# Kernel tuning notes

Measured on AMD Instinct MI355X. Metric: run time of the kernel, lower is better.

Reference implementation:

```python
import jax, jax.numpy as jnp
import numpy as np

B, T, D, H, O = 128, 1024, 256, 512, 256


def setup_inputs() -> dict:
    key = jax.random.key(0)
    ks = jax.random.split(key, 7)
    s = lambda k, shape, fan: jax.random.normal(k, shape, dtype=jnp.float32) / np.sqrt(fan)
    return {
        "x": jax.random.normal(ks[0], (B, T, D), dtype=jnp.float32),
        "W_ih": s(ks[1], (4 * H, D), D),
        "W_hh": s(ks[2], (4 * H, H), H),
        "b_ih": jnp.zeros((4 * H,), dtype=jnp.float32),
        "b_hh": jnp.zeros((4 * H,), dtype=jnp.float32),
        "W_out": s(ks[5], (O, H), H),
        "b_out": jnp.zeros((O,), dtype=jnp.float32),
    }


def reference(x, W_ih, W_hh, b_ih, b_hh, W_out, b_out):
    Bsz = x.shape[0]
    Hd = W_hh.shape[1]
    # Precompute input projections for all timesteps: [B, T, 4H]
    x_proj = jnp.einsum("btd,gd->btg", x, W_ih) + b_ih + b_hh

    def step(carry, xp_t):
        h, c = carry
        gates = xp_t + h @ W_hh.T  # [B, 4H]
        i, f, g, o = jnp.split(gates, 4, axis=-1)
        i = jax.nn.sigmoid(i)
        f = jax.nn.sigmoid(f)
        g = jnp.tanh(g)
        o = jax.nn.sigmoid(o)
        c = f * c + i * g
        h = o * jnp.tanh(c)
        return (h, c), None

    h0 = jnp.zeros((Bsz, Hd), dtype=x.dtype)
    c0 = jnp.zeros((Bsz, Hd), dtype=x.dtype)
    (h_T, _), _ = jax.lax.scan(step, (h0, c0), jnp.swapaxes(x_proj, 0, 1))
    return h_T @ W_out.T + b_out
```

## Files before the change

kernel.cpp:

```cpp
#include <hip/hip_runtime.h>

#define Bsz 128
#define Tlen 1024
#define Din 256
#define Hdim 512

#define NBG 8
#define NCG 16

typedef __attribute__((ext_vector_type(8))) short short8;
typedef __attribute__((ext_vector_type(4))) float f32x4;
typedef __attribute__((ext_vector_type(4))) unsigned short ushort4_;
typedef __attribute__((ext_vector_type(4))) unsigned int uint4v;

#define HBT_BYTES ((size_t)2 * NBG * 16 * Hdim * 4)
#define HT_OFF ((size_t)524288)
#define XB_OFF ((size_t)786432)
#define XB_BYTES ((size_t)Bsz * Tlen * Din * 2)

__device__ inline unsigned short f2bf(float f) {
    unsigned int u = __builtin_bit_cast(unsigned int, f);
    unsigned int lsb = (u >> 16) & 1u;
    u += 0x7fffu + lsb;
    return (unsigned short)(u >> 16);
}
__device__ inline float sigm_f(float x) { return 1.f / (1.f + __expf(-x)); }
__device__ inline float tanh_f(float x) { return 1.f - 2.f / (__expf(2.f * x) + 1.f); }

__device__ __forceinline__ bool chunk_ok(uint4v v, unsigned want) {
    unsigned m =
        ((v[0] ^ want) | (v[1] ^ want) | (v[2] ^ want) | (v[3] ^ want)) & 0xFFFFu;
    return m == 0;
}
__device__ __forceinline__ void chunk_to_lds(uint4v v, int c, unsigned char* h_lds) {
    int row = c >> 7;
    unsigned lo = (v[0] >> 16) | (v[1] & 0xFFFF0000u);
    unsigned hi = (v[2] >> 16) | (v[3] & 0xFFFF0000u);
    int a = ((row << 10) + ((c & 127) << 3)) ^ ((row & 7) << 4);
    *(unsigned long long*)(h_lds + a) =
        (unsigned long long)lo | ((unsigned long long)hi << 32);
}

__global__ __launch_bounds__(256) void xconv(const float* __restrict__ x,
                                             unsigned short* __restrict__ xb) {
    const size_t nthreads = (size_t)2048 * 256;
#pragma unroll
    for (int it = 0; it < 8; ++it) {
        size_t base =
            ((size_t)blockIdx.x * 256 + threadIdx.x + it * nthreads) * 8;
        float4 a = *(const float4*)(x + base);
        float4 b = *(const float4*)(x + base + 4);
        short8 o;
        o[0] = (short)f2bf(a.x); o[1] = (short)f2bf(a.y);
        o[2] = (short)f2bf(a.z); o[3] = (short)f2bf(a.w);
        o[4] = (short)f2bf(b.x); o[5] = (short)f2bf(b.y);
        o[6] = (short)f2bf(b.z); o[7] = (short)f2bf(b.w);
        *(short8*)(xb + base) = o;
    }
}

template <bool XB>
__global__ __launch_bounds__(512, 1) void lstm_persist_t(
    const float* __restrict__ x, const unsigned short* __restrict__ xb,
    const float* __restrict__ Wih, const float* __restrict__ Whh,
    const float* __restrict__ bih, const float* __restrict__ bhh,
    unsigned int* __restrict__ hbt, float* __restrict__ hT) {
    __shared__ unsigned char h_lds[16 * 1024];
    __shared__ unsigned char xh_lds[2 * 8192];
    __shared__ float gates_w[8][16 * 17];

    const int tid = threadIdx.x;
    const int bid = blockIdx.x;
    const int bg = bid & 7;
    const int cg = bid >> 3;
    const int lane = tid & 63;
    const int w = tid >> 6;
    const int n15 = lane & 15;
    const int k8 = lane >> 4;
    const int grow = bg * 16;
    const int gc = n15 & 3;
    const int gsel = n15 >> 2;
    const int myb = k8 * 4 + gsel;
    const int mycol = cg * 32 + w * 4 + gc;
    const int R = (n15 >> 2) * Hdim + mycol;

    short8 whh[16], wihh[8];
    {
        const float* wr = Whh + (size_t)R * Hdim;
#pragma unroll
        for (int kc = 0; kc < 16; kc++) {
            const float* p = wr + kc * 32 + k8 * 8;
            short8 f;
#pragma unroll
            for (int e = 0; e < 8; e++) f[e] = (short)f2bf(p[e]);
            whh[kc] = f;
        }
        const float* wr2 = Wih + (size_t)R * Din;
#pragma unroll
        for (int kc = 0; kc < 8; kc++) {
            const float* p = wr2 + kc * 32 + k8 * 8;
            short8 f;
#pragma unroll
            for (int e = 0; e < 8; e++) f[e] = (short)f2bf(p[e]);
            wihh[kc] = f;
        }
    }
    float bias4[4];
#pragma unroll
    for (int g = 0; g < 4; g++) bias4[g] = bih[g * Hdim + mycol] + bhh[g * Hdim + mycol];

    const int xrow = XB ? (tid >> 5) : 0;
    const int xc8 = XB ? (tid & 31) : 0;
    short8 xr8;
    float4 xrf[2];

    if (XB) {
        const unsigned short* xrowp = xb + ((size_t)(grow + xrow) * Tlen) * Din;
        short8 v = *(const short8*)(xrowp + (size_t)0 * Din + xc8 * 8);
        int a = ((xrow << 9) + (xc8 << 4)) ^ ((xrow & 7) << 4);
        *(short8*)(xh_lds + a) = v;
        xr8 = *(const short8*)(xrowp + (size_t)1 * Din + xc8 * 8);
    } else {
        const float* xbase = x + (size_t)grow * (Tlen * Din);
#pragma unroll
        for (int i = 0; i < 2; i++) {
            int cidx = tid + i * 512;
            int row = cidx >> 6;
            int c4 = cidx & 63;
            float4 v = *(const float4*)(xbase + (size_t)row * (Tlen * Din) + c4 * 4);
            ushort4_ vh;
            vh[0] = f2bf(v.x); vh[1] = f2bf(v.y); vh[2] = f2bf(v.z); vh[3] = f2bf(v.w);
            int a = ((row << 9) + (c4 << 3)) ^ ((row & 7) << 4);
            *(ushort4_*)(xh_lds + a) = vh;
        }
#pragma unroll
        for (int i = 0; i < 2; i++) {
            int cidx = tid + i * 512;
            int row = cidx >> 6;
            int c4 = cidx & 63;
            xrf[i] = *(const float4*)(xbase + (size_t)row * (Tlen * Din) + Din + c4 * 4);
        }
    }
    __syncthreads();

    float c_reg = 0.f, h_last = 0.f;

    for (int t = 0; t < Tlen; ++t) {
        if (t + 1 < Tlen) {
            unsigned char* xdst = xh_lds + ((t + 1) & 1) * 8192;
            if (XB) {
                int a = ((xrow << 9) + (xc8 << 4)) ^ ((xrow & 7) << 4);
                *(short8*)(xdst + a) = xr8;
            } else {
#pragma unroll
                for (int i = 0; i < 2; i++) {
                    int cidx = tid + i * 512;
                    int row = cidx >> 6;
                    int c4 = cidx & 63;
                    ushort4_ vh;
                    vh[0] = f2bf(xrf[i].x); vh[1] = f2bf(xrf[i].y);
                    vh[2] = f2bf(xrf[i].z); vh[3] = f2bf(xrf[i].w);
                    int a = ((row << 9) + (c4 << 3)) ^ ((row & 7) << 4);
                    *(ushort4_*)(xdst + a) = vh;
                }
            }
        }

        unsigned char* xh = xh_lds + (t & 1) * 8192;
        f32x4 acc0 = {0.f, 0.f, 0.f, 0.f}, acc1 = {0.f, 0.f, 0.f, 0.f};
#pragma unroll
        for (int kc = 0; kc < 8; kc++) {
            int a = (((n15 << 9) + (kc << 6) + (k8 << 4)) ^ ((n15 & 7) << 4));
            short8 xv = *(const short8*)(xh + a);
            if (kc & 1)
                acc1 = __builtin_amdgcn_mfma_f32_16x16x32_bf16(xv, wihh[kc], acc1, 0, 0, 0);
            else
                acc0 = __builtin_amdgcn_mfma_f32_16x16x32_bf16(xv, wihh[kc], acc0, 0, 0, 0);
        }

        if (t > 0) {
            const unsigned int* hb = hbt + ((size_t)(t & 1) * NBG + bg) * 8192;
            const unsigned int* p0 = hb + (size_t)tid * 4;
            const unsigned int* p1 = hb + (size_t)(tid + 512) * 4;
            const unsigned int* p2 = hb + (size_t)(tid + 1024) * 4;
            const unsigned int* p3 = hb + (size_t)(tid + 1536) * 4;
            uint4v r0, r1, r2, r3;
            asm volatile(
                "global_load_dwordx4 %0, %4, off sc0 sc1\n\t"
                "global_load_dwordx4 %1, %5, off sc0 sc1\n\t"
                "global_load_dwordx4 %2, %6, off sc0 sc1\n\t"
                "global_load_dwordx4 %3, %7, off sc0 sc1"
                : "=&v"(r0), "=&v"(r1), "=&v"(r2), "=&v"(r3)
                : "v"(p0), "v"(p1), "v"(p2), "v"(p3)
                : "memory");
            const unsigned want = (unsigned)t;
            asm volatile("s_waitcnt vmcnt(0)" ::: "memory");
            __builtin_amdgcn_sched_barrier(0);
            unsigned need = 0;
            if (chunk_ok(r0, want)) chunk_to_lds(r0, tid, h_lds); else need |= 1u;
            if (chunk_ok(r1, want)) chunk_to_lds(r1, tid + 512, h_lds); else need |= 2u;
            if (chunk_ok(r2, want)) chunk_to_lds(r2, tid + 1024, h_lds); else need |= 4u;
            if (chunk_ok(r3, want)) chunk_to_lds(r3, tid + 1536, h_lds); else need |= 8u;
            int rounds = 0;
            while (need && ++rounds < (1 << 14)) {
                if (rounds > 6) __builtin_amdgcn_s_sleep(1);
                if (need & 1u)
                    asm volatile("global_load_dwordx4 %0, %1, off sc0 sc1"
                                 : "=&v"(r0) : "v"(p0) : "memory");
                if (need & 2u)
                    asm volatile("global_load_dwordx4 %0, %1, off sc0 sc1"
                                 : "=&v"(r1) : "v"(p1) : "memory");
                if (need & 4u)
                    asm volatile("global_load_dwordx4 %0, %1, off sc0 sc1"
                                 : "=&v"(r2) : "v"(p2) : "memory");
                if (need & 8u)
                    asm volatile("global_load_dwordx4 %0, %1, off sc0 sc1"
                                 : "=&v"(r3) : "v"(p3) : "memory");
                asm volatile("s_waitcnt vmcnt(0)" ::: "memory");
                __builtin_amdgcn_sched_barrier(0);
                if ((need & 1u) && chunk_ok(r0, want)) { chunk_to_lds(r0, tid, h_lds); need &= ~1u; }
                if ((need & 2u) && chunk_ok(r1, want)) { chunk_to_lds(r1, tid + 512, h_lds); need &= ~2u; }
                if ((need & 4u) && chunk_ok(r2, want)) { chunk_to_lds(r2, tid + 1024, h_lds); need &= ~4u; }
                if ((need & 8u) && chunk_ok(r3, want)) { chunk_to_lds(r3, tid + 1536, h_lds); need &= ~8u; }
            }
        } else {
#pragma unroll
            for (int i = 0; i < 4; i++) {
                int c = tid + i * 512;
                int row = c >> 7;
                int a = ((row << 10) + ((c & 127) << 3)) ^ ((row & 7) << 4);
                *(unsigned long long*)(h_lds + a) = 0ULL;
            }
        }
        asm volatile("s_waitcnt lgkmcnt(0)" ::: "memory");
        __builtin_amdgcn_s_barrier();
        __builtin_amdgcn_sched_barrier(0);

#pragma unroll
        for (int kc = 0; kc < 16; kc++) {
            short8 a = *(const short8*)(h_lds + (((n15 << 10) + (kc << 6) + (k8 << 4)) ^
                                                ((n15 & 7) << 4)));
            if (kc & 1)
                acc1 = __builtin_amdgcn_mfma_f32_16x16x32_bf16(a, whh[kc], acc1, 0, 0, 0);
            else
                acc0 = __builtin_amdgcn_mfma_f32_16x16x32_bf16(a, whh[kc], acc0, 0, 0, 0);
        }

        if (t + 2 < Tlen) {
            if (XB) {
                xr8 = *(const short8*)(xb + ((size_t)(grow + xrow) * Tlen + (t + 2)) * Din +
                                       xc8 * 8);
            } else {
                const float* xbase =
                    x + (size_t)grow * (Tlen * Din) + (size_t)(t + 2) * Din;
#pragma unroll
                for (int i = 0; i < 2; i++) {
                    int cidx = tid + i * 512;
                    int row = cidx >> 6;
                    int c4 = cidx & 63;
                    xrf[i] = *(const float4*)(xbase + (size_t)row * (Tlen * Din) + c4 * 4);
                }
            }
        }

        float* gt = gates_w[w];
#pragma unroll
        for (int j2 = 0; j2 < 4; j2++) gt[(k8 * 4 + j2) * 17 + n15] = acc0[j2] + acc1[j2];
        {
            float pre[4];
#pragma unroll
            for (int g = 0; g < 4; g++) pre[g] = gt[myb * 17 + g * 4 + gc] + bias4[g];
            float ig = sigm_f(pre[0]);
            float fg = sigm_f(pre[1]);
            float gg = tanh_f(pre[2]);
            float og = sigm_f(pre[3]);
            c_reg = fg * c_reg + ig * gg;
            h_last = og * tanh_f(c_reg);
            unsigned int word = ((unsigned int)f2bf(h_last) << 16) | (unsigned)(t + 1);
            unsigned int* dst = hbt + ((size_t)((t + 1) & 1) * NBG + bg) * 8192 +
                                (size_t)myb * Hdim + mycol;
            __hip_atomic_store(dst, word, __ATOMIC_RELAXED, __HIP_MEMORY_SCOPE_AGENT);
        }
        asm volatile("s_waitcnt lgkmcnt(0)" ::: "memory");
        __builtin_amdgcn_s_barrier();
        __builtin_amdgcn_sched_barrier(0);
    }
    hT[(size_t)(grow + myb) * Hdim + mycol] = h_last;
}

__global__ __launch_bounds__(256) void out_proj(const float* __restrict__ hT,
                                                const float* __restrict__ Wout,
                                                const float* __restrict__ bout,
                                                float* __restrict__ out) {
    __shared__ float h_s[16 * 512];
    __shared__ float w_s[64 * 69];
    const int tid = threadIdx.x;
    const int bt = blockIdx.x >> 2;
    const int ot = blockIdx.x & 3;
#pragma unroll
    for (int i = 0; i < 8; i++) {
        int cidx = tid + i * 256;
        int row = cidx >> 7;
        int c4 = cidx & 127;
        *(float4*)(&h_s[row * 512 + c4 * 4]) =
            *(const float4*)(hT + (size_t)(bt * 16 + row) * 512 + c4 * 4);
    }
    const int o = tid & 63;
    const int bq = tid >> 6;
    float acc[4] = {0.f, 0.f, 0.f, 0.f};
    for (int kc = 0; kc < 8; kc++) {
        __syncthreads();
#pragma unroll
        for (int i = 0; i < 4; i++) {
            int cidx = tid + i * 256;
            int row = cidx >> 4;
            int c4 = cidx & 15;
            float4 v = *(const float4*)(Wout + (size_t)(ot * 64 + row) * 512 + kc * 64 +
                                        c4 * 4);
            float* dst = &w_s[row * 69 + c4 * 4];
            dst[0] = v.x;
            dst[1] = v.y;
            dst[2] = v.z;
            dst[3] = v.w;
        }
        __syncthreads();
#pragma unroll 16
        for (int k = 0; k < 64; k++) {
            float wv = w_s[o * 69 + k];
#pragma unroll
            for (int bi = 0; bi < 4; bi++)
                acc[bi] += h_s[(bq * 4 + bi) * 512 + kc * 64 + k] * wv;
        }
    }
    float bo = bout[ot * 64 + o];
#pragma unroll
    for (int bi = 0; bi < 4; bi++)
        out[(size_t)(bt * 16 + bq * 4 + bi) * 256 + ot * 64 + o] = acc[bi] + bo;
}

extern "C" void kernel_launch(void* const* d_in, const int* in_sizes, int n_in,
                              void* d_out, int out_size, void* d_ws, size_t ws_size,
                              hipStream_t stream) {
    const float* x = (const float*)d_in[0];
    const float* Wih = (const float*)d_in[1];
    const float* Whh = (const float*)d_in[2];
    const float* bih = (const float*)d_in[3];
    const float* bhh = (const float*)d_in[4];
    const float* Wout = (const float*)d_in[5];
    const float* bout = (const float*)d_in[6];
    float* out = (float*)d_out;

    char* ws = (char*)d_ws;
    unsigned int* hbt = (unsigned int*)ws;
    float* hT = (float*)(ws + HT_OFF);
    unsigned short* xbuf = (unsigned short*)(ws + XB_OFF);

    hipMemsetAsync(hbt, 0, HBT_BYTES, stream);
    if (ws_size >= XB_OFF + XB_BYTES) {
        xconv<<<dim3(2048), dim3(256), 0, stream>>>(x, xbuf);
        lstm_persist_t<true><<<dim3(NBG * NCG), dim3(512), 0, stream>>>(
            x, xbuf, Wih, Whh, bih, bhh, hbt, hT);
    } else {
        lstm_persist_t<false><<<dim3(NBG * NCG), dim3(512), 0, stream>>>(
            x, (const unsigned short*)nullptr, Wih, Whh, bih, bhh, hbt, hT);
    }
    out_proj<<<dim3(32), dim3(256), 0, stream>>>(hT, Wout, bout, out);
}
```

Before: 2.011 ms.

## Use 1024-thread blocks covering 64 hidden columns, halving persistent block count

```diff
diff --git a/kernel.cpp b/kernel.cpp
--- a/kernel.cpp
+++ b/kernel.cpp
@@ -6,7 +6,7 @@
 #define Hdim 512
 
 #define NBG 8
-#define NCG 16
+#define NCG 8
 
 typedef __attribute__((ext_vector_type(8))) short short8;
 typedef __attribute__((ext_vector_type(4))) float f32x4;
@@ -60,14 +60,14 @@
 }
 
 template <bool XB>
-__global__ __launch_bounds__(512, 1) void lstm_persist_t(
+__global__ __launch_bounds__(1024, 1) void lstm_persist_t(
     const float* __restrict__ x, const unsigned short* __restrict__ xb,
     const float* __restrict__ Wih, const float* __restrict__ Whh,
     const float* __restrict__ bih, const float* __restrict__ bhh,
     unsigned int* __restrict__ hbt, float* __restrict__ hT) {
     __shared__ unsigned char h_lds[16 * 1024];
     __shared__ unsigned char xh_lds[2 * 8192];
-    __shared__ float gates_w[8][16 * 17];
+    __shared__ float gates_w[16][16 * 17];
 
     const int tid = threadIdx.x;
     const int bid = blockIdx.x;
@@ -81,7 +81,7 @@
     const int gc = n15 & 3;
     const int gsel = n15 >> 2;
     const int myb = k8 * 4 + gsel;
-    const int mycol = cg * 32 + w * 4 + gc;
+    const int mycol = cg * 64 + w * 4 + gc;
     const int R = (n15 >> 2) * Hdim + mycol;
 
     short8 whh[16], wihh[8];
@@ -109,37 +109,23 @@
 #pragma unroll
     for (int g = 0; g < 4; g++) bias4[g] = bih[g * Hdim + mycol] + bhh[g * Hdim + mycol];
 
-    const int xrow = XB ? (tid >> 5) : 0;
-    const int xc8 = XB ? (tid & 31) : 0;
-    short8 xr8;
-    float4 xrf[2];
+    const int xrow = tid >> 6;
+    const int xc4 = tid & 63;
+    const int xa = ((xrow << 9) + (xc4 << 3)) ^ ((xrow & 7) << 4);
+    ushort4_ xr4;
+    float4 xrf;
 
     if (XB) {
-        const unsigned short* xrowp = xb + ((size_t)(grow + xrow) * Tlen) * Din;
-        short8 v = *(const short8*)(xrowp + (size_t)0 * Din + xc8 * 8);
-        int a = ((xrow << 9) + (xc8 << 4)) ^ ((xrow & 7) << 4);
-        *(short8*)(xh_lds + a) = v;
-        xr8 = *(const short8*)(xrowp + (size_t)1 * Din + xc8 * 8);
+        const unsigned short* xrowp = xb + (size_t)(grow + xrow) * Tlen * Din;
+        *(ushort4_*)(xh_lds + xa) = *(const ushort4_*)(xrowp + xc4 * 4);
+        xr4 = *(const ushort4_*)(xrowp + Din + xc4 * 4);
     } else {
-        const float* xbase = x + (size_t)grow * (Tlen * Din);
-#pragma unroll
-        for (int i = 0; i < 2; i++) {
-            int cidx = tid + i * 512;
-            int row = cidx >> 6;
-            int c4 = cidx & 63;
-            float4 v = *(const float4*)(xbase + (size_t)row * (Tlen * Din) + c4 * 4);
-            ushort4_ vh;
-            vh[0] = f2bf(v.x); vh[1] = f2bf(v.y); vh[2] = f2bf(v.z); vh[3] = f2bf(v.w);
-            int a = ((row << 9) + (c4 << 3)) ^ ((row & 7) << 4);
-            *(ushort4_*)(xh_lds + a) = vh;
-        }
-#pragma unroll
-        for (int i = 0; i < 2; i++) {
-            int cidx = tid + i * 512;
-            int row = cidx >> 6;
-            int c4 = cidx & 63;
-            xrf[i] = *(const float4*)(xbase + (size_t)row * (Tlen * Din) + Din + c4 * 4);
-        }
+        const float* xrowp = x + (size_t)(grow + xrow) * Tlen * Din;
+        float4 v = *(const float4*)(xrowp + xc4 * 4);
+        ushort4_ vh;
+        vh[0] = f2bf(v.x); vh[1] = f2bf(v.y); vh[2] = f2bf(v.z); vh[3] = f2bf(v.w);
+        *(ushort4_*)(xh_lds + xa) = vh;
+        xrf = *(const float4*)(xrowp + Din + xc4 * 4);
     }
     __syncthreads();
 
@@ -149,20 +135,12 @@
         if (t + 1 < Tlen) {
             unsigned char* xdst = xh_lds + ((t + 1) & 1) * 8192;
             if (XB) {
-                int a = ((xrow << 9) + (xc8 << 4)) ^ ((xrow & 7) << 4);
-                *(short8*)(xdst + a) = xr8;
+                *(ushort4_*)(xdst + xa) = xr4;
             } else {
-#pragma unroll
-                for (int i = 0; i < 2; i++) {
-                    int cidx = tid + i * 512;
-                    int row = cidx >> 6;
-                    int c4 = cidx & 63;
-                    ushort4_ vh;
-                    vh[0] = f2bf(xrf[i].x); vh[1] = f2bf(xrf[i].y);
-                    vh[2] = f2bf(xrf[i].z); vh[3] = f2bf(xrf[i].w);
-                    int a = ((row << 9) + (c4 << 3)) ^ ((row & 7) << 4);
-                    *(ushort4_*)(xdst + a) = vh;
-                }
+                ushort4_ vh;
+                vh[0] = f2bf(xrf.x); vh[1] = f2bf(xrf.y);
+                vh[2] = f2bf(xrf.z); vh[3] = f2bf(xrf.w);
+                *(ushort4_*)(xdst + xa) = vh;
             }
         }
 
@@ -181,28 +159,22 @@
         if (t > 0) {
             const unsigned int* hb = hbt + ((size_t)(t & 1) * NBG + bg) * 8192;
             const unsigned int* p0 = hb + (size_t)tid * 4;
-            const unsigned int* p1 = hb + (size_t)(tid + 512) * 4;
-            const unsigned int* p2 = hb + (size_t)(tid + 1024) * 4;
-            const unsigned int* p3 = hb + (size_t)(tid + 1536) * 4;
-            uint4v r0, r1, r2, r3;
+            const unsigned int* p1 = hb + (size_t)(tid + 1024) * 4;
+            uint4v r0, r1;
             asm volatile(
-                "global_load_dwordx4 %0, %4, off sc0 sc1\n\t"
-                "global_load_dwordx4 %1, %5, off sc0 sc1\n\t"
-                "global_load_dwordx4 %2, %6, off sc0 sc1\n\t"
-                "global_load_dwordx4 %3, %7, off sc0 sc1"
-                : "=&v"(r0), "=&v"(r1), "=&v"(r2), "=&v"(r3)
-                : "v"(p0), "v"(p1), "v"(p2), "v"(p3)
+                "global_load_dwordx4 %0, %2, off sc0 sc1\n\t"
+                "global_load_dwordx4 %1, %3, off sc0 sc1"
+                : "=&v"(r0), "=&v"(r1)
+                : "v"(p0), "v"(p1)
                 : "memory");
             const unsigned want = (unsigned)t;
             asm volatile("s_waitcnt vmcnt(0)" ::: "memory");
             __builtin_amdgcn_sched_barrier(0);
             unsigned need = 0;
             if (chunk_ok(r0, want)) chunk_to_lds(r0, tid, h_lds); else need |= 1u;
-            if (chunk_ok(r1, want)) chunk_to_lds(r1, tid + 512, h_lds); else need |= 2u;
-            if (chunk_ok(r2, want)) chunk_to_lds(r2, tid + 1024, h_lds); else need |= 4u;
-            if (chunk_ok(r3, want)) chunk_to_lds(r3, tid + 1536, h_lds); else need |= 8u;
+            if (chunk_ok(r1, want)) chunk_to_lds(r1, tid + 1024, h_lds); else need |= 2u;
             int rounds = 0;
-            while (need && ++rounds < (1 << 14)) {
+            while (need && ++rounds < (1 << 15)) {
                 if (rounds > 6) __builtin_amdgcn_s_sleep(1);
                 if (need & 1u)
                     asm volatile("global_load_dwordx4 %0, %1, off sc0 sc1"
@@ -210,23 +182,15 @@
                 if (need & 2u)
                     asm volatile("global_load_dwordx4 %0, %1, off sc0 sc1"
                                  : "=&v"(r1) : "v"(p1) : "memory");
-                if (need & 4u)
-                    asm volatile("global_load_dwordx4 %0, %1, off sc0 sc1"
-                                 : "=&v"(r2) : "v"(p2) : "memory");
-                if (need & 8u)
-                    asm volatile("global_load_dwordx4 %0, %1, off sc0 sc1"
-                                 : "=&v"(r3) : "v"(p3) : "memory");
                 asm volatile("s_waitcnt vmcnt(0)" ::: "memory");
                 __builtin_amdgcn_sched_barrier(0);
                 if ((need & 1u) && chunk_ok(r0, want)) { chunk_to_lds(r0, tid, h_lds); need &= ~1u; }
-                if ((need & 2u) && chunk_ok(r1, want)) { chunk_to_lds(r1, tid + 512, h_lds); need &= ~2u; }
-                if ((need & 4u) && chunk_ok(r2, want)) { chunk_to_lds(r2, tid + 1024, h_lds); need &= ~4u; }
-                if ((need & 8u) && chunk_ok(r3, want)) { chunk_to_lds(r3, tid + 1536, h_lds); need &= ~8u; }
+                if ((need & 2u) && chunk_ok(r1, want)) { chunk_to_lds(r1, tid + 1024, h_lds); need &= ~2u; }
             }
         } else {
 #pragma unroll
-            for (int i = 0; i < 4; i++) {
-                int c = tid + i * 512;
+            for (int i = 0; i < 2; i++) {
+                int c = tid + i * 1024;
                 int row = c >> 7;
                 int a = ((row << 10) + ((c & 127) << 3)) ^ ((row & 7) << 4);
                 *(unsigned long long*)(h_lds + a) = 0ULL;
@@ -248,18 +212,11 @@
 
         if (t + 2 < Tlen) {
             if (XB) {
-                xr8 = *(const short8*)(xb + ((size_t)(grow + xrow) * Tlen + (t + 2)) * Din +
-                                       xc8 * 8);
+                xr4 = *(const ushort4_*)(xb + ((size_t)(grow + xrow) * Tlen + (t + 2)) * Din +
+                                         xc4 * 4);
             } else {
-                const float* xbase =
-                    x + (size_t)grow * (Tlen * Din) + (size_t)(t + 2) * Din;
-#pragma unroll
-                for (int i = 0; i < 2; i++) {
-                    int cidx = tid + i * 512;
-                    int row = cidx >> 6;
-                    int c4 = cidx & 63;
-                    xrf[i] = *(const float4*)(xbase + (size_t)row * (Tlen * Din) + c4 * 4);
-                }
+                xrf = *(const float4*)(x + ((size_t)(grow + xrow) * Tlen + (t + 2)) * Din +
+                                       xc4 * 4);
             }
         }
 
@@ -358,10 +315,10 @@
     hipMemsetAsync(hbt, 0, HBT_BYTES, stream);
     if (ws_size >= XB_OFF + XB_BYTES) {
         xconv<<<dim3(2048), dim3(256), 0, stream>>>(x, xbuf);
-        lstm_persist_t<true><<<dim3(NBG * NCG), dim3(512), 0, stream>>>(
+        lstm_persist_t<true><<<dim3(NBG * NCG), dim3(1024), 0, stream>>>(
             x, xbuf, Wih, Whh, bih, bhh, hbt, hT);
     } else {
-        lstm_persist_t<false><<<dim3(NBG * NCG), dim3(512), 0, stream>>>(
+        lstm_persist_t<false><<<dim3(NBG * NCG), dim3(1024), 0, stream>>>(
             x, (const unsigned short*)nullptr, Wih, Whh, bih, bhh, hbt, hT);
     }
     out_proj<<<dim3(32), dim3(256), 0, stream>>>(hT, Wout, bout, out);
```

Measured after the change: 5.366 ms. 167% more time.

## Duplicate hidden-state exchange into L2-scoped and system-scoped buffers with fallback polling

Applied to the files above, without the earlier changes.

```diff
diff --git a/kernel.cpp b/kernel.cpp
--- a/kernel.cpp
+++ b/kernel.cpp
@@ -14,8 +14,9 @@
 typedef __attribute__((ext_vector_type(4))) unsigned int uint4v;
 
 #define HBT_BYTES ((size_t)2 * NBG * 16 * Hdim * 4)
-#define HT_OFF ((size_t)524288)
-#define XB_OFF ((size_t)786432)
+#define HBTG_OFF ((size_t)524288)
+#define HT_OFF ((size_t)1048576)
+#define XB_OFF ((size_t)1310720)
 #define XB_BYTES ((size_t)Bsz * Tlen * Din * 2)
 
 __device__ inline unsigned short f2bf(float f) {
@@ -64,7 +65,8 @@
     const float* __restrict__ x, const unsigned short* __restrict__ xb,
     const float* __restrict__ Wih, const float* __restrict__ Whh,
     const float* __restrict__ bih, const float* __restrict__ bhh,
-    unsigned int* __restrict__ hbt, float* __restrict__ hT) {
+    unsigned int* __restrict__ hbtL, unsigned int* __restrict__ hbtG,
+    float* __restrict__ hT) {
     __shared__ unsigned char h_lds[16 * 1024];
     __shared__ unsigned char xh_lds[2 * 8192];
     __shared__ float gates_w[8][16 * 17];
@@ -144,6 +146,7 @@
     __syncthreads();
 
     float c_reg = 0.f, h_last = 0.f;
+    int useLocal = 1;
 
     for (int t = 0; t < Tlen; ++t) {
         if (t + 1 < Tlen) {
@@ -179,20 +182,35 @@
         }
 
         if (t > 0) {
-            const unsigned int* hb = hbt + ((size_t)(t & 1) * NBG + bg) * 8192;
-            const unsigned int* p0 = hb + (size_t)tid * 4;
-            const unsigned int* p1 = hb + (size_t)(tid + 512) * 4;
-            const unsigned int* p2 = hb + (size_t)(tid + 1024) * 4;
-            const unsigned int* p3 = hb + (size_t)(tid + 1536) * 4;
+            const size_t pbase = ((size_t)(t & 1) * NBG + bg) * 8192;
+            const unsigned int* pL0 = hbtL + pbase + (size_t)tid * 4;
+            const unsigned int* pL1 = hbtL + pbase + (size_t)(tid + 512) * 4;
+            const unsigned int* pL2 = hbtL + pbase + (size_t)(tid + 1024) * 4;
+            const unsigned int* pL3 = hbtL + pbase + (size_t)(tid + 1536) * 4;
+            const unsigned int* pG0 = hbtG + pbase + (size_t)tid * 4;
+            const unsigned int* pG1 = hbtG + pbase + (size_t)(tid + 512) * 4;
+            const unsigned int* pG2 = hbtG + pbase + (size_t)(tid + 1024) * 4;
+            const unsigned int* pG3 = hbtG + pbase + (size_t)(tid + 1536) * 4;
             uint4v r0, r1, r2, r3;
-            asm volatile(
-                "global_load_dwordx4 %0, %4, off sc0 sc1\n\t"
-                "global_load_dwordx4 %1, %5, off sc0 sc1\n\t"
-                "global_load_dwordx4 %2, %6, off sc0 sc1\n\t"
-                "global_load_dwordx4 %3, %7, off sc0 sc1"
-                : "=&v"(r0), "=&v"(r1), "=&v"(r2), "=&v"(r3)
-                : "v"(p0), "v"(p1), "v"(p2), "v"(p3)
-                : "memory");
+            if (useLocal) {
+                asm volatile(
+                    "global_load_dwordx4 %0, %4, off sc0\n\t"
+                    "global_load_dwordx4 %1, %5, off sc0\n\t"
+                    "global_load_dwordx4 %2, %6, off sc0\n\t"
+                    "global_load_dwordx4 %3, %7, off sc0"
+                    : "=&v"(r0), "=&v"(r1), "=&v"(r2), "=&v"(r3)
+                    : "v"(pL0), "v"(pL1), "v"(pL2), "v"(pL3)
+                    : "memory");
+            } else {
+                asm volatile(
+                    "global_load_dwordx4 %0, %4, off sc0 sc1\n\t"
+                    "global_load_dwordx4 %1, %5, off sc0 sc1\n\t"
+                    "global_load_dwordx4 %2, %6, off sc0 sc1\n\t"
+                    "global_load_dwordx4 %3, %7, off sc0 sc1"
+                    : "=&v"(r0), "=&v"(r1), "=&v"(r2), "=&v"(r3)
+                    : "v"(pG0), "v"(pG1), "v"(pG2), "v"(pG3)
+                    : "memory");
+            }
             const unsigned want = (unsigned)t;
             asm volatile("s_waitcnt vmcnt(0)" ::: "memory");
             __builtin_amdgcn_sched_barrier(0);
@@ -202,20 +220,36 @@
             if (chunk_ok(r2, want)) chunk_to_lds(r2, tid + 1024, h_lds); else need |= 4u;
             if (chunk_ok(r3, want)) chunk_to_lds(r3, tid + 1536, h_lds); else need |= 8u;
             int rounds = 0;
-            while (need && ++rounds < (1 << 14)) {
-                if (rounds > 6) __builtin_amdgcn_s_sleep(1);
-                if (need & 1u)
-                    asm volatile("global_load_dwordx4 %0, %1, off sc0 sc1"
-                                 : "=&v"(r0) : "v"(p0) : "memory");
-                if (need & 2u)
-                    asm volatile("global_load_dwordx4 %0, %1, off sc0 sc1"
-                                 : "=&v"(r1) : "v"(p1) : "memory");
-                if (need & 4u)
-                    asm volatile("global_load_dwordx4 %0, %1, off sc0 sc1"
-                                 : "=&v"(r2) : "v"(p2) : "memory");
-                if (need & 8u)
-                    asm volatile("global_load_dwordx4 %0, %1, off sc0 sc1"
-                                 : "=&v"(r3) : "v"(p3) : "memory");
+            while (need && ++rounds < (1 << 15)) {
+                if (useLocal && rounds > 12) useLocal = 0;
+                if (rounds > 16) __builtin_amdgcn_s_sleep(1);
+                if (useLocal) {
+                    if (need & 1u)
+                        asm volatile("global_load_dwordx4 %0, %1, off sc0"
+                                     : "=&v"(r0) : "v"(pL0) : "memory");
+                    if (need & 2u)
+                        asm volatile("global_load_dwordx4 %0, %1, off sc0"
+                                     : "=&v"(r1) : "v"(pL1) : "memory");
+                    if (need & 4u)
+                        asm volatile("global_load_dwordx4 %0, %1, off sc0"
+                                     : "=&v"(r2) : "v"(pL2) : "memory");
+                    if (need & 8u)
+                        asm volatile("global_load_dwordx4 %0, %1, off sc0"
+                                     : "=&v"(r3) : "v"(pL3) : "memory");
+                } else {
+                    if (need & 1u)
+                        asm volatile("global_load_dwordx4 %0, %1, off sc0 sc1"
+                                     : "=&v"(r0) : "v"(pG0) : "memory");
+                    if (need & 2u)
+                        asm volatile("global_load_dwordx4 %0, %1, off sc0 sc1"
+                                     : "=&v"(r1) : "v"(pG1) : "memory");
+                    if (need & 4u)
+                        asm volatile("global_load_dwordx4 %0, %1, off sc0 sc1"
+                                     : "=&v"(r2) : "v"(pG2) : "memory");
+                    if (need & 8u)
+                        asm volatile("global_load_dwordx4 %0, %1, off sc0 sc1"
+                                     : "=&v"(r3) : "v"(pG3) : "memory");
+                }
                 asm volatile("s_waitcnt vmcnt(0)" ::: "memory");
                 __builtin_amdgcn_sched_barrier(0);
                 if ((need & 1u) && chunk_ok(r0, want)) { chunk_to_lds(r0, tid, h_lds); need &= ~1u; }
@@ -277,9 +311,14 @@
             c_reg = fg * c_reg + ig * gg;
             h_last = og * tanh_f(c_reg);
             unsigned int word = ((unsigned int)f2bf(h_last) << 16) | (unsigned)(t + 1);
-            unsigned int* dst = hbt + ((size_t)((t + 1) & 1) * NBG + bg) * 8192 +
-                                (size_t)myb * Hdim + mycol;
-            __hip_atomic_store(dst, word, __ATOMIC_RELAXED, __HIP_MEMORY_SCOPE_AGENT);
+            size_t off = ((size_t)((t + 1) & 1) * NBG + bg) * 8192 +
+                         (size_t)myb * Hdim + mycol;
+            unsigned int* dstL = hbtL + off;
+            unsigned int* dstG = hbtG + off;
+            asm volatile("global_store_dword %0, %1, off sc0" ::"v"(dstL), "v"(word)
+                         : "memory");
+            asm volatile("global_store_dword %0, %1, off sc0 sc1" ::"v"(dstG), "v"(word)
+                         : "memory");
         }
         asm volatile("s_waitcnt lgkmcnt(0)" ::: "memory");
         __builtin_amdgcn_s_barrier();
@@ -351,18 +390,19 @@
     float* out = (float*)d_out;
 
     char* ws = (char*)d_ws;
-    unsigned int* hbt = (unsigned int*)ws;
+    unsigned int* hbtL = (unsigned int*)ws;
+    unsigned int* hbtG = (unsigned int*)(ws + HBTG_OFF);
     float* hT = (float*)(ws + HT_OFF);
     unsigned short* xbuf = (unsigned short*)(ws + XB_OFF);
 
-    hipMemsetAsync(hbt, 0, HBT_BYTES, stream);
+    hipMemsetAsync(ws, 0, 2 * HBT_BYTES, stream);
     if (ws_size >= XB_OFF + XB_BYTES) {
         xconv<<<dim3(2048), dim3(256), 0, stream>>>(x, xbuf);
         lstm_persist_t<true><<<dim3(NBG * NCG), dim3(512), 0, stream>>>(
-            x, xbuf, Wih, Whh, bih, bhh, hbt, hT);
+            x, xbuf, Wih, Whh, bih, bhh, hbtL, hbtG, hT);
     } else {
         lstm_persist_t<false><<<dim3(NBG * NCG), dim3(512), 0, stream>>>(
-            x, (const unsigned short*)nullptr, Wih, Whh, bih, bhh, hbt, hT);
+            x, (const unsigned short*)nullptr, Wih, Whh, bih, bhh, hbtL, hbtG, hT);
     }
     out_proj<<<dim3(32), dim3(256), 0, stream>>>(hT, Wout, bout, out);
 }
```

Result: slower. 2.672 ms (+32.9%).

## Interleave two batch groups per workgroup to overlap hidden-state polling with compute

Applied to the files above, without the earlier changes.

```diff
diff --git a/kernel.cpp b/kernel.cpp
--- a/kernel.cpp
+++ b/kernel.cpp
@@ -7,6 +7,7 @@
 
 #define NBG 8
 #define NCG 16
+#define NWG 64
 
 typedef __attribute__((ext_vector_type(8))) short short8;
 typedef __attribute__((ext_vector_type(4))) float f32x4;
@@ -41,13 +42,56 @@
         (unsigned long long)lo | ((unsigned long long)hi << 32);
 }
 
+__device__ __forceinline__ void validate_fill(uint4v& r0, uint4v& r1, uint4v& r2,
+                                              uint4v& r3, const unsigned int* p0,
+                                              const unsigned int* p1,
+                                              const unsigned int* p2,
+                                              const unsigned int* p3, unsigned want,
+                                              int tid, unsigned char* h_lds) {
+    unsigned need = 0;
+    if (chunk_ok(r0, want)) chunk_to_lds(r0, tid, h_lds); else need |= 1u;
+    if (chunk_ok(r1, want)) chunk_to_lds(r1, tid + 512, h_lds); else need |= 2u;
+    if (chunk_ok(r2, want)) chunk_to_lds(r2, tid + 1024, h_lds); else need |= 4u;
+    if (chunk_ok(r3, want)) chunk_to_lds(r3, tid + 1536, h_lds); else need |= 8u;
+    int rounds = 0;
+    while (need && ++rounds < (1 << 15)) {
+        if (rounds > 8) __builtin_amdgcn_s_sleep(1);
+        if (need & 1u)
+            asm volatile("global_load_dwordx4 %0, %1, off sc0 sc1"
+                         : "=&v"(r0) : "v"(p0) : "memory");
+        if (need & 2u)
+            asm volatile("global_load_dwordx4 %0, %1, off sc0 sc1"
+                         : "=&v"(r1) : "v"(p1) : "memory");
+        if (need & 4u)
+            asm volatile("global_load_dwordx4 %0, %1, off sc0 sc1"
+                         : "=&v"(r2) : "v"(p2) : "memory");
+        if (need & 8u)
+            asm volatile("global_load_dwordx4 %0, %1, off sc0 sc1"
+                         : "=&v"(r3) : "v"(p3) : "memory");
+        asm volatile("s_waitcnt vmcnt(0)" ::: "memory");
+        __builtin_amdgcn_sched_barrier(0);
+        if ((need & 1u) && chunk_ok(r0, want)) { chunk_to_lds(r0, tid, h_lds); need &= ~1u; }
+        if ((need & 2u) && chunk_ok(r1, want)) { chunk_to_lds(r1, tid + 512, h_lds); need &= ~2u; }
+        if ((need & 4u) && chunk_ok(r2, want)) { chunk_to_lds(r2, tid + 1024, h_lds); need &= ~4u; }
+        if ((need & 8u) && chunk_ok(r3, want)) { chunk_to_lds(r3, tid + 1536, h_lds); need &= ~8u; }
+    }
+}
+
+#define SWEEP_ISSUE(r0, r1, r2, r3, p0, p1, p2, p3)                 \
+    asm volatile("global_load_dwordx4 %0, %4, off sc0 sc1\n\t"      \
+                 "global_load_dwordx4 %1, %5, off sc0 sc1\n\t"      \
+                 "global_load_dwordx4 %2, %6, off sc0 sc1\n\t"      \
+                 "global_load_dwordx4 %3, %7, off sc0 sc1"          \
+                 : "=&v"(r0), "=&v"(r1), "=&v"(r2), "=&v"(r3)       \
+                 : "v"(p0), "v"(p1), "v"(p2), "v"(p3)               \
+                 : "memory")
+
 __global__ __launch_bounds__(256) void xconv(const float* __restrict__ x,
                                              unsigned short* __restrict__ xb) {
     const size_t nthreads = (size_t)2048 * 256;
 #pragma unroll
     for (int it = 0; it < 8; ++it) {
-        size_t base =
-            ((size_t)blockIdx.x * 256 + threadIdx.x + it * nthreads) * 8;
+        size_t base = ((size_t)blockIdx.x * 256 + threadIdx.x + it * nthreads) * 8;
         float4 a = *(const float4*)(x + base);
         float4 b = *(const float4*)(x + base + 4);
         short8 o;
@@ -60,24 +104,26 @@
 }
 
 template <bool XB>
-__global__ __launch_bounds__(512, 1) void lstm_persist_t(
+__global__ __launch_bounds__(512, 1) void lstm_pair(
     const float* __restrict__ x, const unsigned short* __restrict__ xb,
     const float* __restrict__ Wih, const float* __restrict__ Whh,
     const float* __restrict__ bih, const float* __restrict__ bhh,
     unsigned int* __restrict__ hbt, float* __restrict__ hT) {
     __shared__ unsigned char h_lds[16 * 1024];
-    __shared__ unsigned char xh_lds[2 * 8192];
+    __shared__ unsigned char xA_lds[2 * 8192];
+    __shared__ unsigned char xB_lds[2 * 8192];
     __shared__ float gates_w[8][16 * 17];
 
     const int tid = threadIdx.x;
-    const int bid = blockIdx.x;
-    const int bg = bid & 7;
-    const int cg = bid >> 3;
+    const int wg = blockIdx.x;
+    const int cg = wg >> 2;
+    const int pr = wg & 3;
+    const int bgA = pr * 2, bgB = pr * 2 + 1;
+    const int growA = bgA * 16, growB = bgB * 16;
     const int lane = tid & 63;
     const int w = tid >> 6;
     const int n15 = lane & 15;
     const int k8 = lane >> 4;
-    const int grow = bg * 16;
     const int gc = n15 & 3;
     const int gsel = n15 >> 2;
     const int myb = k8 * 4 + gsel;
@@ -109,120 +155,60 @@
 #pragma unroll
     for (int g = 0; g < 4; g++) bias4[g] = bih[g * Hdim + mycol] + bhh[g * Hdim + mycol];
 
-    const int xrow = XB ? (tid >> 5) : 0;
-    const int xc8 = XB ? (tid & 31) : 0;
-    short8 xr8;
-    float4 xrf[2];
+    const int xrow = tid >> 5, xc8 = tid & 31;
+    const int xa = ((xrow << 9) + (xc8 << 4)) ^ ((xrow & 7) << 4);
+    short8 xrA8, xrB8;
+    float4 xfA, xfB;
+    float4 xfA2, xfB2;
 
     if (XB) {
-        const unsigned short* xrowp = xb + ((size_t)(grow + xrow) * Tlen) * Din;
-        short8 v = *(const short8*)(xrowp + (size_t)0 * Din + xc8 * 8);
-        int a = ((xrow << 9) + (xc8 << 4)) ^ ((xrow & 7) << 4);
-        *(short8*)(xh_lds + a) = v;
-        xr8 = *(const short8*)(xrowp + (size_t)1 * Din + xc8 * 8);
+        const unsigned short* xpA = xb + (size_t)(growA + xrow) * Tlen * Din;
+        const unsigned short* xpB = xb + (size_t)(growB + xrow) * Tlen * Din;
+        *(short8*)(xA_lds + xa) = *(const short8*)(xpA + xc8 * 8);
+        *(short8*)(xB_lds + xa) = *(const short8*)(xpB + xc8 * 8);
+        xrA8 = *(const short8*)(xpA + Din + xc8 * 8);
+        xrB8 = *(const short8*)(xpB + Din + xc8 * 8);
     } else {
-        const float* xbase = x + (size_t)grow * (Tlen * Din);
-#pragma unroll
-        for (int i = 0; i < 2; i++) {
-            int cidx = tid + i * 512;
-            int row = cidx >> 6;
-            int c4 = cidx & 63;
-            float4 v = *(const float4*)(xbase + (size_t)row * (Tlen * Din) + c4 * 4);
-            ushort4_ vh;
-            vh[0] = f2bf(v.x); vh[1] = f2bf(v.y); vh[2] = f2bf(v.z); vh[3] = f2bf(v.w);
-            int a = ((row << 9) + (c4 << 3)) ^ ((row & 7) << 4);
-            *(ushort4_*)(xh_lds + a) = vh;
-        }
-#pragma unroll
-        for (int i = 0; i < 2; i++) {
-            int cidx = tid + i * 512;
-            int row = cidx >> 6;
-            int c4 = cidx & 63;
-            xrf[i] = *(const float4*)(xbase + (size_t)row * (Tlen * Din) + Din + c4 * 4);
-        }
+        const float* xpA = x + (size_t)(growA + xrow) * Tlen * Din;
+        const float* xpB = x + (size_t)(growB + xrow) * Tlen * Din;
+        float4 a0 = *(const float4*)(xpA + xc8 * 8);
+        float4 a1 = *(const float4*)(xpA + xc8 * 8 + 4);
+        float4 b0 = *(const float4*)(xpB + xc8 * 8);
+        float4 b1 = *(const float4*)(xpB + xc8 * 8 + 4);
+        short8 oa, ob;
+        oa[0]=(short)f2bf(a0.x); oa[1]=(short)f2bf(a0.y); oa[2]=(short)f2bf(a0.z); oa[3]=(short)f2bf(a0.w);
+        oa[4]=(short)f2bf(a1.x); oa[5]=(short)f2bf(a1.y); oa[6]=(short)f2bf(a1.z); oa[7]=(short)f2bf(a1.w);
+        ob[0]=(short)f2bf(b0.x); ob[1]=(short)f2bf(b0.y); ob[2]=(short)f2bf(b0.z); ob[3]=(short)f2bf(b0.w);
+        ob[4]=(short)f2bf(b1.x); ob[5]=(short)f2bf(b1.y); ob[6]=(short)f2bf(b1.z); ob[7]=(short)f2bf(b1.w);
+        *(short8*)(xA_lds + xa) = oa;
+        *(short8*)(xB_lds + xa) = ob;
+        xfA = *(const float4*)(xpA + Din + xc8 * 8);
+        xfA2 = *(const float4*)(xpA + Din + xc8 * 8 + 4);
+        xfB = *(const float4*)(xpB + Din + xc8 * 8);
+        xfB2 = *(const float4*)(xpB + Din + xc8 * 8 + 4);
     }
     __syncthreads();
 
-    float c_reg = 0.f, h_last = 0.f;
+    float cA = 0.f, hAv = 0.f, cB = 0.f, hBv = 0.f;
+    uint4v sA0, sA1, sA2, sA3, sB0, sB1, sB2, sB3;
 
     for (int t = 0; t < Tlen; ++t) {
-        if (t + 1 < Tlen) {
-            unsigned char* xdst = xh_lds + ((t + 1) & 1) * 8192;
-            if (XB) {
-                int a = ((xrow << 9) + (xc8 << 4)) ^ ((xrow & 7) << 4);
-                *(short8*)(xdst + a) = xr8;
-            } else {
-#pragma unroll
-                for (int i = 0; i < 2; i++) {
-                    int cidx = tid + i * 512;
-                    int row = cidx >> 6;
-                    int c4 = cidx & 63;
-                    ushort4_ vh;
-                    vh[0] = f2bf(xrf[i].x); vh[1] = f2bf(xrf[i].y);
-                    vh[2] = f2bf(xrf[i].z); vh[3] = f2bf(xrf[i].w);
-                    int a = ((row << 9) + (c4 << 3)) ^ ((row & 7) << 4);
-                    *(ushort4_*)(xdst + a) = vh;
-                }
-            }
-        }
-
-        unsigned char* xh = xh_lds + (t & 1) * 8192;
-        f32x4 acc0 = {0.f, 0.f, 0.f, 0.f}, acc1 = {0.f, 0.f, 0.f, 0.f};
-#pragma unroll
-        for (int kc = 0; kc < 8; kc++) {
-            int a = (((n15 << 9) + (kc << 6) + (k8 << 4)) ^ ((n15 & 7) << 4));
-            short8 xv = *(const short8*)(xh + a);
-            if (kc & 1)
-                acc1 = __builtin_amdgcn_mfma_f32_16x16x32_bf16(xv, wihh[kc], acc1, 0, 0, 0);
-            else
-                acc0 = __builtin_amdgcn_mfma_f32_16x16x32_bf16(xv, wihh[kc], acc0, 0, 0, 0);
-        }
+        const size_t pbA = ((size_t)(t & 1) * NBG + bgA) * 8192;
+        const size_t pbB = ((size_t)(t & 1) * NBG + bgB) * 8192;
+        const unsigned int* pA0 = hbt + pbA + (size_t)tid * 4;
+        const unsigned int* pA1 = hbt + pbA + (size_t)(tid + 512) * 4;
+        const unsigned int* pA2 = hbt + pbA + (size_t)(tid + 1024) * 4;
+        const unsigned int* pA3 = hbt + pbA + (size_t)(tid + 1536) * 4;
+        const unsigned int* pB0 = hbt + pbB + (size_t)tid * 4;
+        const unsigned int* pB1 = hbt + pbB + (size_t)(tid + 512) * 4;
+        const unsigned int* pB2 = hbt + pbB + (size_t)(tid + 1024) * 4;
+        const unsigned int* pB3 = hbt + pbB + (size_t)(tid + 1536) * 4;
 
         if (t > 0) {
-            const unsigned int* hb = hbt + ((size_t)(t & 1) * NBG + bg) * 8192;
-            const unsigned int* p0 = hb + (size_t)tid * 4;
-            const unsigned int* p1 = hb + (size_t)(tid + 512) * 4;
-            const unsigned int* p2 = hb + (size_t)(tid + 1024) * 4;
-            const unsigned int* p3 = hb + (size_t)(tid + 1536) * 4;
-            uint4v r0, r1, r2, r3;
-            asm volatile(
-                "global_load_dwordx4 %0, %4, off sc0 sc1\n\t"
-                "global_load_dwordx4 %1, %5, off sc0 sc1\n\t"
-                "global_load_dwordx4 %2, %6, off sc0 sc1\n\t"
-                "global_load_dwordx4 %3, %7, off sc0 sc1"
-                : "=&v"(r0), "=&v"(r1), "=&v"(r2), "=&v"(r3)
-                : "v"(p0), "v"(p1), "v"(p2), "v"(p3)
-                : "memory");
-            const unsigned want = (unsigned)t;
-            asm volatile("s_waitcnt vmcnt(0)" ::: "memory");
-            __builtin_amdgcn_sched_barrier(0);
-            unsigned need = 0;
-            if (chunk_ok(r0, want)) chunk_to_lds(r0, tid, h_lds); else need |= 1u;
-            if (chunk_ok(r1, want)) chunk_to_lds(r1, tid + 512, h_lds); else need |= 2u;
-            if (chunk_ok(r2, want)) chunk_to_lds(r2, tid + 1024, h_lds); else need |= 4u;
-            if (chunk_ok(r3, want)) chunk_to_lds(r3, tid + 1536, h_lds); else need |= 8u;
-            int rounds = 0;
-            while (need && ++rounds < (1 << 14)) {
-                if (rounds > 6) __builtin_amdgcn_s_sleep(1);
-                if (need & 1u)
-                    asm volatile("global_load_dwordx4 %0, %1, off sc0 sc1"
-                                 : "=&v"(r0) : "v"(p0) : "memory");
-                if (need & 2u)
-                    asm volatile("global_load_dwordx4 %0, %1, off sc0 sc1"
-                                 : "=&v"(r1) : "v"(p1) : "memory");
-                if (need & 4u)
-                    asm volatile("global_load_dwordx4 %0, %1, off sc0 sc1"
-                                 : "=&v"(r2) : "v"(p2) : "memory");
-                if (need & 8u)
-                    asm volatile("global_load_dwordx4 %0, %1, off sc0 sc1"
-                                 : "=&v"(r3) : "v"(p3) : "memory");
-                asm volatile("s_waitcnt vmcnt(0)" ::: "memory");
-                __builtin_amdgcn_sched_barrier(0);
-                if ((need & 1u) && chunk_ok(r0, want)) { chunk_to_lds(r0, tid, h_lds); need &= ~1u; }
-                if ((need & 2u) && chunk_ok(r1, want)) { chunk_to_lds(r1, tid + 512, h_lds); need &= ~2u; }
-                if ((need & 4u) && chunk_ok(r2, want)) { chunk_to_lds(r2, tid + 1024, h_lds); need &= ~4u; }
-                if ((need & 8u) && chunk_ok(r3, want)) { chunk_to_lds(r3, tid + 1536, h_lds); need &= ~8u; }
-            }
+            asm volatile("s_waitcnt vmcnt(1)" ::: "memory");
+            __builtin_amdgcn_sched_barrier(0);
+            validate_fill(sA0, sA1, sA2, sA3, pA0, pA1, pA2, pA3, (unsigned)t, tid,
+                          h_lds);
         } else {
 #pragma unroll
             for (int i = 0; i < 4; i++) {
@@ -236,37 +222,53 @@
         __builtin_amdgcn_s_barrier();
         __builtin_amdgcn_sched_barrier(0);
 
-#pragma unroll
-        for (int kc = 0; kc < 16; kc++) {
-            short8 a = *(const short8*)(h_lds + (((n15 << 10) + (kc << 6) + (k8 << 4)) ^
-                                                ((n15 & 7) << 4)));
-            if (kc & 1)
-                acc1 = __builtin_amdgcn_mfma_f32_16x16x32_bf16(a, whh[kc], acc1, 0, 0, 0);
-            else
-                acc0 = __builtin_amdgcn_mfma_f32_16x16x32_bf16(a, whh[kc], acc0, 0, 0, 0);
-        }
-
-        if (t + 2 < Tlen) {
-            if (XB) {
-                xr8 = *(const short8*)(xb + ((size_t)(grow + xrow) * Tlen + (t + 2)) * Din +
-                                       xc8 * 8);
-            } else {
-                const float* xbase =
-                    x + (size_t)grow * (Tlen * Din) + (size_t)(t + 2) * Din;
-#pragma unroll
-                for (int i = 0; i < 2; i++) {
-                    int cidx = tid + i * 512;
-                    int row = cidx >> 6;
-                    int c4 = cidx & 63;
-                    xrf[i] = *(const float4*)(xbase + (size_t)row * (Tlen * Din) + c4 * 4);
+        {
+            unsigned char* xh = xA_lds + (t & 1) * 8192;
+            f32x4 acc0 = {0.f, 0.f, 0.f, 0.f}, acc1 = {0.f, 0.f, 0.f, 0.f};
+#pragma unroll
+            for (int kc = 0; kc < 8; kc++) {
+                int a = (((n15 << 9) + (kc << 6) + (k8 << 4)) ^ ((n15 & 7) << 4));
+                short8 xv = *(const short8*)(xh + a);
+                if (kc & 1)
+                    acc1 = __builtin_amdgcn_mfma_f32_16x16x32_bf16(xv, wihh[kc], acc1, 0, 0, 0);
+                else
+                    acc0 = __builtin_amdgcn_mfma_f32_16x16x32_bf16(xv, wihh[kc], acc0, 0, 0, 0);
+            }
+            __builtin_amdgcn_sched_barrier(0);
+            if (t > 0) SWEEP_ISSUE(sB0, sB1, sB2, sB3, pB0, pB1, pB2, pB3);
+            __builtin_amdgcn_sched_barrier(0);
+#pragma unroll
+            for (int kc = 0; kc < 16; kc++) {
+                short8 a = *(const short8*)(h_lds + (((n15 << 10) + (kc << 6) + (k8 << 4)) ^
+                                                    ((n15 & 7) << 4)));
+                if (kc & 1)
+                    acc1 = __builtin_amdgcn_mfma_f32_16x16x32_bf16(a, whh[kc], acc1, 0, 0, 0);
+                else
+                    acc0 = __builtin_amdgcn_mfma_f32_16x16x32_bf16(a, whh[kc], acc0, 0, 0, 0);
+            }
+            if (t + 1 < Tlen) {
+                unsigned char* xdst = xA_lds + ((t + 1) & 1) * 8192;
+                if (XB) {
+                    *(short8*)(xdst + xa) = xrA8;
+                } else {
+                    short8 o;
+                    o[0]=(short)f2bf(xfA.x); o[1]=(short)f2bf(xfA.y); o[2]=(short)f2bf(xfA.z); o[3]=(short)f2bf(xfA.w);
+                    o[4]=(short)f2bf(xfA2.x); o[5]=(short)f2bf(xfA2.y); o[6]=(short)f2bf(xfA2.z); o[7]=(short)f2bf(xfA2.w);
+                    *(short8*)(xdst + xa) = o;
                 }
             }
-        }
-
-        float* gt = gates_w[w];
-#pragma unroll
-        for (int j2 = 0; j2 < 4; j2++) gt[(k8 * 4 + j2) * 17 + n15] = acc0[j2] + acc1[j2];
-        {
+            if (t + 2 < Tlen) {
+                if (XB) {
+                    xrA8 = *(const short8*)(xb + ((size_t)(growA + xrow) * Tlen + (t + 2)) * Din + xc8 * 8);
+                } else {
+                    const float* s = x + ((size_t)(growA + xrow) * Tlen + (t + 2)) * Din + xc8 * 8;
+                    xfA = *(const float4*)s;
+                    xfA2 = *(const float4*)(s + 4);
+                }
+            }
+            float* gt = gates_w[w];
+#pragma unroll
+            for (int j2 = 0; j2 < 4; j2++) gt[(k8 * 4 + j2) * 17 + n15] = acc0[j2] + acc1[j2];
             float pre[4];
 #pragma unroll
             for (int g = 0; g < 4; g++) pre[g] = gt[myb * 17 + g * 4 + gc] + bias4[g];
@@ -274,18 +276,116 @@
             float fg = sigm_f(pre[1]);
             float gg = tanh_f(pre[2]);
             float og = sigm_f(pre[3]);
-            c_reg = fg * c_reg + ig * gg;
-            h_last = og * tanh_f(c_reg);
-            unsigned int word = ((unsigned int)f2bf(h_last) << 16) | (unsigned)(t + 1);
-            unsigned int* dst = hbt + ((size_t)((t + 1) & 1) * NBG + bg) * 8192 +
-                                (size_t)myb * Hdim + mycol;
-            __hip_atomic_store(dst, word, __ATOMIC_RELAXED, __HIP_MEMORY_SCOPE_AGENT);
+            cA = fg * cA + ig * gg;
+            hAv = og * tanh_f(cA);
+            if (t + 1 < Tlen) {
+                unsigned int word = ((unsigned int)f2bf(hAv) << 16) | (unsigned)(t + 1);
+                unsigned int* dst = hbt + ((size_t)((t + 1) & 1) * NBG + bgA) * 8192 +
+                                    (size_t)myb * Hdim + mycol;
+                __builtin_amdgcn_sched_barrier(0);
+                asm volatile("global_store_dword %0, %1, off sc0 sc1" ::"v"(dst),
+                             "v"(word)
+                             : "memory");
+                __builtin_amdgcn_sched_barrier(0);
+            }
         }
         asm volatile("s_waitcnt lgkmcnt(0)" ::: "memory");
         __builtin_amdgcn_s_barrier();
         __builtin_amdgcn_sched_barrier(0);
-    }
-    hT[(size_t)(grow + myb) * Hdim + mycol] = h_last;
+
+        if (t > 0) {
+            if (t + 1 < Tlen)
+                asm volatile("s_waitcnt vmcnt(1)" ::: "memory");
+            else
+                asm volatile("s_waitcnt vmcnt(0)" ::: "memory");
+            __builtin_amdgcn_sched_barrier(0);
+            validate_fill(sB0, sB1, sB2, sB3, pB0, pB1, pB2, pB3, (unsigned)t, tid,
+                          h_lds);
+        }
+        asm volatile("s_waitcnt lgkmcnt(0)" ::: "memory");
+        __builtin_amdgcn_s_barrier();
+        __builtin_amdgcn_sched_barrier(0);
+
+        {
+            unsigned char* xh = xB_lds + (t & 1) * 8192;
+            f32x4 acc0 = {0.f, 0.f, 0.f, 0.f}, acc1 = {0.f, 0.f, 0.f, 0.f};
+#pragma unroll
+            for (int kc = 0; kc < 8; kc++) {
+                int a = (((n15 << 9) + (kc << 6) + (k8 << 4)) ^ ((n15 & 7) << 4));
+                short8 xv = *(const short8*)(xh + a);
+                if (kc & 1)
+                    acc1 = __builtin_amdgcn_mfma_f32_16x16x32_bf16(xv, wihh[kc], acc1, 0, 0, 0);
+                else
+                    acc0 = __builtin_amdgcn_mfma_f32_16x16x32_bf16(xv, wihh[kc], acc0, 0, 0, 0);
+            }
+            __builtin_amdgcn_sched_barrier(0);
+            if (t + 1 < Tlen) {
+                const size_t nbA = ((size_t)((t + 1) & 1) * NBG + bgA) * 8192;
+                SWEEP_ISSUE(sA0, sA1, sA2, sA3, hbt + nbA + (size_t)tid * 4,
+                            hbt + nbA + (size_t)(tid + 512) * 4,
+                            hbt + nbA + (size_t)(tid + 1024) * 4,
+                            hbt + nbA + (size_t)(tid + 1536) * 4);
+            }
+            __builtin_amdgcn_sched_barrier(0);
+#pragma unroll
+            for (int kc = 0; kc < 16; kc++) {
+                short8 a = *(const short8*)(h_lds + (((n15 << 10) + (kc << 6) + (k8 << 4)) ^
+                                                    ((n15 & 7) << 4)));
+                if (kc & 1)
+                    acc1 = __builtin_amdgcn_mfma_f32_16x16x32_bf16(a, whh[kc], acc1, 0, 0, 0);
+                else
+                    acc0 = __builtin_amdgcn_mfma_f32_16x16x32_bf16(a, whh[kc], acc0, 0, 0, 0);
+            }
+            if (t + 1 < Tlen) {
+                unsigned char* xdst = xB_lds + ((t + 1) & 1) * 8192;
+                if (XB) {
+                    *(short8*)(xdst + xa) = xrB8;
+                } else {
+                    short8 o;
+                    o[0]=(short)f2bf(xfB.x); o[1]=(short)f2bf(xfB.y); o[2]=(short)f2bf(xfB.z); o[3]=(short)f2bf(xfB.w);
+                    o[4]=(short)f2bf(xfB2.x); o[5]=(short)f2bf(xfB2.y); o[6]=(short)f2bf(xfB2.z); o[7]=(short)f2bf(xfB2.w);
+                    *(short8*)(xdst + xa) = o;
+                }
+            }
+            if (t + 2 < Tlen) {
+                if (XB) {
+                    xrB8 = *(const short8*)(xb + ((size_t)(growB + xrow) * Tlen + (t + 2)) * Din + xc8 * 8);
+                } else {
+                    const float* s = x + ((size_t)(growB + xrow) * Tlen + (t + 2)) * Din + xc8 * 8;
+                    xfB = *(const float4*)s;
+                    xfB2 = *(const float4*)(s + 4);
+                }
+            }
+            float* gt = gates_w[w];
+#pragma unroll
+            for (int j2 = 0; j2 < 4; j2++) gt[(k8 * 4 + j2) * 17 + n15] = acc0[j2] + acc1[j2];
+            float pre[4];
+#pragma unroll
+            for (int g = 0; g < 4; g++) pre[g] = gt[myb * 17 + g * 4 + gc] + bias4[g];
+            float ig = sigm_f(pre[0]);
+            float fg = sigm_f(pre[1]);
+            float gg = tanh_f(pre[2]);
+            float og = sigm_f(pre[3]);
+            cB = fg * cB + ig * gg;
+            hBv = og * tanh_f(cB);
+            if (t + 1 < Tlen) {
+                unsigned int word = ((unsigned int)f2bf(hBv) << 16) | (unsigned)(t + 1);
+                unsigned int* dst = hbt + ((size_t)((t + 1) & 1) * NBG + bgB) * 8192 +
+                                    (size_t)myb * Hdim + mycol;
+                __builtin_amdgcn_sched_barrier(0);
+                asm volatile("global_store_dword %0, %1, off sc0 sc1" ::"v"(dst),
+                             "v"(word)
+                             : "memory");
+                __builtin_amdgcn_sched_barrier(0);
+            }
+        }
+        asm volatile("s_waitcnt lgkmcnt(0)" ::: "memory");
+        __builtin_amdgcn_s_barrier();
+        __builtin_amdgcn_sched_barrier(0);
+    }
+
+    hT[(size_t)(growA + myb) * Hdim + mycol] = hAv;
+    hT[(size_t)(growB + myb) * Hdim + mycol] = hBv;
 }
 
 __global__ __launch_bounds__(256) void out_proj(const float* __restrict__ hT,
@@ -358,10 +458,10 @@
     hipMemsetAsync(hbt, 0, HBT_BYTES, stream);
     if (ws_size >= XB_OFF + XB_BYTES) {
         xconv<<<dim3(2048), dim3(256), 0, stream>>>(x, xbuf);
-        lstm_persist_t<true><<<dim3(NBG * NCG), dim3(512), 0, stream>>>(
-            x, xbuf, Wih, Whh, bih, bhh, hbt, hT);
+        lstm_pair<true><<<dim3(NWG), dim3(512), 0, stream>>>(x, xbuf, Wih, Whh, bih,
+                                                             bhh, hbt, hT);
     } else {
-        lstm_persist_t<false><<<dim3(NBG * NCG), dim3(512), 0, stream>>>(
+        lstm_pair<false><<<dim3(NWG), dim3(512), 0, stream>>>(
             x, (const unsigned short*)nullptr, Wih, Whh, bih, bhh, hbt, hT);
     }
     out_proj<<<dim3(32), dim3(256), 0, stream>>>(hT, Wout, bout, out);
```

Result: slower. 3.094 ms (+53.9%).
